# Optimization experiments

Hardware: AMD Instinct MI355X
Metric: run time of the kernel (lower is better)

The kernel has to match this reference:

```python
import jax, jax.numpy as jnp
import numpy as np

N = 100000
E = 600000
IN_DIM = 128
OUT_DIM = 256
BN_EPS = 1e-5


def setup_inputs() -> dict:
    key = jax.random.key(0)
    ks = jax.random.split(key, 12)
    x = jax.random.normal(ks[0], (N, IN_DIM), dtype=jnp.float32)
    edge_index = jax.random.randint(ks[1], (2, E), 0, N, dtype=jnp.int64)
    s1 = 1.0 / np.sqrt(IN_DIM)
    s2 = 1.0 / np.sqrt(OUT_DIM)
    return {
        "x": x,
        "edge_index": edge_index,
        "eps": jnp.zeros((), dtype=jnp.float32),  # GINConv eps init = 0
        "W1": jax.random.uniform(ks[2], (IN_DIM, OUT_DIM), jnp.float32, -s1, s1),
        "b1": jnp.zeros((OUT_DIM,), jnp.float32),
        "W2": jax.random.uniform(ks[3], (OUT_DIM, OUT_DIM), jnp.float32, -s2, s2),
        "b2": jnp.zeros((OUT_DIM,), jnp.float32),
        "gamma": jnp.ones((OUT_DIM,), jnp.float32),
        "beta": jnp.zeros((OUT_DIM,), jnp.float32),
        "run_mean": jnp.zeros((OUT_DIM,), jnp.float32),
        "run_var": jnp.ones((OUT_DIM,), jnp.float32),
        "Wp": jax.random.uniform(ks[4], (IN_DIM, OUT_DIM), jnp.float32, -s1, s1),
        "bp": jnp.zeros((OUT_DIM,), jnp.float32),
    }


def reference(x, edge_index, eps, W1, b1, W2, b2, gamma, beta, run_mean, run_var, Wp, bp):
    src, dst = edge_index[0], edge_index[1]
    # GIN aggregation: sum_{j in N(i)} x_j  (scatter-add of source features to dst)
    agg = jax.ops.segment_sum(x[src], dst, num_segments=N)
    h = (1.0 + eps) * x + agg            # [N, in_dim]
    # 2-layer MLP (nn1)
    h = jax.nn.relu(h @ W1 + b1) @ W2 + b2   # [N, out_dim]
    # BatchNorm1d (eval mode: running stats); dropout = identity (eval)
    h = (h - run_mean) * jax.lax.rsqrt(run_var + BN_EPS) * gamma + beta
    # residual with projection (in_dim != out_dim)
    return h + x @ Wp + bp
```

## Files before the change

kernel.cpp:

```cpp
#include <hip/hip_runtime.h>

#define N_ 100000
#define E_ 600000
#define IND_ 128
#define OUTD_ 256
#define NT_ (N_/16)
#define NB_ 98
#define CASTN_ (N_*IND_/2)

typedef __attribute__((ext_vector_type(8))) short bf16x8;
typedef __attribute__((ext_vector_type(4))) float f32x4;
typedef __attribute__((ext_vector_type(2))) unsigned int u32x2;

static __device__ __forceinline__ unsigned f2bf_u(float f){
  union { float f; unsigned u; } v; v.f = f;
  return (v.u + 0x7fffu + ((v.u >> 16) & 1u)) >> 16;
}
static __device__ __forceinline__ unsigned pack2(float a, float b){
  return f2bf_u(a) | (f2bf_u(b) << 16);
}
static __device__ __forceinline__ float blo(unsigned u){
  union { unsigned u; float f; } v; v.u = u << 16; return v.f;
}
static __device__ __forceinline__ float bhi(unsigned u){
  union { unsigned u; float f; } v; v.u = u & 0xffff0000u; return v.f;
}
static __device__ __forceinline__ void gload_lds16(const bf16x8* g, bf16x8* l){
  __builtin_amdgcn_global_load_lds((const __attribute__((address_space(1))) void*)g,
                                   (__attribute__((address_space(3))) void*)l, 16, 0, 0);
}

__global__ void k_prep(const float* __restrict__ x,
                       const float* __restrict__ W1, const float* __restrict__ W2,
                       const float* __restrict__ Wp, const float* __restrict__ b2,
                       const float* __restrict__ gamma, const float* __restrict__ beta,
                       const float* __restrict__ mean, const float* __restrict__ var,
                       const float* __restrict__ bp,
                       const int* __restrict__ dst, int* __restrict__ deg,
                       unsigned short* __restrict__ W1s, unsigned short* __restrict__ W2s,
                       unsigned short* __restrict__ Wps,
                       float* __restrict__ scale, float* __restrict__ shift,
                       unsigned* __restrict__ xbw)
{
  int gid = blockIdx.x*256 + threadIdx.x;
  if (gid < 16384) {
    const float* W; unsigned short* Ws; int u;
    if (gid < 4096)       { W = W1; Ws = W1s; u = gid; }
    else if (gid < 12288) { W = W2; Ws = W2s; u = gid - 4096; }
    else                  { W = Wp; Ws = Wps; u = gid - 12288; }
    int l  = u & 63;
    int km = (u >> 6) & 1;
    int t  = (u >> 7) & 15;
    int q  = u >> 11;
    int kk = 2*q + km;
    int kb = kk*32 + (l >> 4)*8;
    int c  = 16*t + (l & 15);
    #pragma unroll
    for (int j = 0; j < 8; j++)
      Ws[u*8 + j] = (unsigned short)f2bf_u(W[(size_t)(kb + j)*OUTD_ + c]);
  } else if (gid < 16640) {
    int c = gid - 16384;
    float s = gamma[c] * rsqrtf(var[c] + 1e-5f);
    scale[c] = s;
    shift[c] = (b2[c] - mean[c]) * s + beta[c] + bp[c];
  } else if (gid < 16640 + CASTN_) {
    int ci = gid - 16640;
    float2 v = ((const float2*)x)[ci];
    xbw[ci] = pack2(v.x, v.y);
  } else if (gid < 16640 + CASTN_ + E_) {
    int e = gid - 16640 - CASTN_;
    atomicAdd(&deg[dst[e]], 1);
  }
}

__global__ __launch_bounds__(1024) void k_scan1(const int* __restrict__ deg,
                                                int* __restrict__ bsum, int* __restrict__ offs){
  __shared__ int red[16];
  int tid = threadIdx.x;
  int i = blockIdx.x*1024 + tid;
  int v = (i < N_) ? deg[i] : 0;
  #pragma unroll
  for (int d = 32; d; d >>= 1) v += __shfl_down(v, d);
  if ((tid & 63) == 0) red[tid >> 6] = v;
  __syncthreads();
  if (tid < 16) {
    int s = red[tid];
    #pragma unroll
    for (int d = 8; d; d >>= 1) s += __shfl_down(s, d, 16);
    if (tid == 0) bsum[blockIdx.x] = s;
  }
  if (blockIdx.x == 0 && tid == 0) offs[N_] = E_;
}

__global__ __launch_bounds__(1024) void k_scan2(const int* __restrict__ deg,
                                                const int* __restrict__ bsum, int* __restrict__ offs){
  __shared__ int bs[128];
  __shared__ int d1[1024];
  int tid = threadIdx.x;
  if (tid < 128) bs[tid] = (tid < NB_) ? bsum[tid] : 0;
  __syncthreads();
  #pragma unroll
  for (int d = 1; d < 128; d <<= 1){
    int v = (tid < 128 && tid >= d) ? bs[tid - d] : 0;
    __syncthreads();
    if (tid < 128) bs[tid] += v;
    __syncthreads();
  }
  int bprefix = (blockIdx.x > 0) ? bs[blockIdx.x - 1] : 0;
  int i = blockIdx.x*1024 + tid;
  int v = (i < N_) ? deg[i] : 0;
  d1[tid] = v;
  __syncthreads();
  #pragma unroll
  for (int d = 1; d < 1024; d <<= 1){
    int t = (tid >= d) ? d1[tid - d] : 0;
    __syncthreads();
    d1[tid] += t;
    __syncthreads();
  }
  if (i < N_) offs[i] = bprefix + d1[tid] - v;
}

__global__ void k_fill(const int* __restrict__ src, const int* __restrict__ dst,
                       const int* __restrict__ offs, int* __restrict__ cur, int* __restrict__ adj){
  int e = blockIdx.x*256 + threadIdx.x;
  if (e < E_) {
    int d = dst[e];
    int p = atomicAdd(&cur[d], 1);
    adj[offs[d] + p] = src[e];
  }
}

__global__ void k_agg(const unsigned* __restrict__ xb32, const int* __restrict__ offs,
                      const int* __restrict__ adj, const float* __restrict__ epsp,
                      unsigned* __restrict__ h0)
{
  int row  = blockIdx.x*4 + (threadIdx.x >> 6);
  int lane = threadIdx.x & 63;
  if (row >= N_) return;
  unsigned xw = xb32[(size_t)row*64 + lane];
  float ax0=0,ay0=0,ax1=0,ay1=0,ax2=0,ay2=0,ax3=0,ay3=0;
  float ax4=0,ay4=0,ax5=0,ay5=0,ax6=0,ay6=0,ax7=0,ay7=0;
  int b = offs[row], e = offs[row+1];
  for (int base = b; base < e; base += 64){
    int cnt = min(64, e - base);
    int idx = adj[base + min(lane, cnt - 1)];
    int j = 0;
    for (; j + 8 <= cnt; j += 8){
      int n0 = __shfl(idx, j+0), n1 = __shfl(idx, j+1);
      int n2 = __shfl(idx, j+2), n3 = __shfl(idx, j+3);
      int n4 = __shfl(idx, j+4), n5 = __shfl(idx, j+5);
      int n6 = __shfl(idx, j+6), n7 = __shfl(idx, j+7);
      unsigned v0 = xb32[(size_t)n0*64 + lane];
      unsigned v1 = xb32[(size_t)n1*64 + lane];
      unsigned v2 = xb32[(size_t)n2*64 + lane];
      unsigned v3 = xb32[(size_t)n3*64 + lane];
      unsigned v4 = xb32[(size_t)n4*64 + lane];
      unsigned v5 = xb32[(size_t)n5*64 + lane];
      unsigned v6 = xb32[(size_t)n6*64 + lane];
      unsigned v7 = xb32[(size_t)n7*64 + lane];
      ax0 += blo(v0); ay0 += bhi(v0);
      ax1 += blo(v1); ay1 += bhi(v1);
      ax2 += blo(v2); ay2 += bhi(v2);
      ax3 += blo(v3); ay3 += bhi(v3);
      ax4 += blo(v4); ay4 += bhi(v4);
      ax5 += blo(v5); ay5 += bhi(v5);
      ax6 += blo(v6); ay6 += bhi(v6);
      ax7 += blo(v7); ay7 += bhi(v7);
    }
    for (; j + 4 <= cnt; j += 4){
      int n0 = __shfl(idx, j+0), n1 = __shfl(idx, j+1);
      int n2 = __shfl(idx, j+2), n3 = __shfl(idx, j+3);
      unsigned v0 = xb32[(size_t)n0*64 + lane];
      unsigned v1 = xb32[(size_t)n1*64 + lane];
      unsigned v2 = xb32[(size_t)n2*64 + lane];
      unsigned v3 = xb32[(size_t)n3*64 + lane];
      ax0 += blo(v0); ay0 += bhi(v0);
      ax1 += blo(v1); ay1 += bhi(v1);
      ax2 += blo(v2); ay2 += bhi(v2);
      ax3 += blo(v3); ay3 += bhi(v3);
    }
    if (j + 2 <= cnt){
      int n0 = __shfl(idx, j+0), n1 = __shfl(idx, j+1);
      unsigned v0 = xb32[(size_t)n0*64 + lane];
      unsigned v1 = xb32[(size_t)n1*64 + lane];
      ax4 += blo(v0); ay4 += bhi(v0);
      ax5 += blo(v1); ay5 += bhi(v1);
      j += 2;
    }
    if (j < cnt){
      int n = __shfl(idx, j);
      unsigned v = xb32[(size_t)n*64 + lane];
      ax6 += blo(v); ay6 += bhi(v);
    }
  }
  float ax = ((ax0+ax1)+(ax2+ax3)) + ((ax4+ax5)+(ax6+ax7));
  float ay = ((ay0+ay1)+(ay2+ay3)) + ((ay4+ay5)+(ay6+ay7));
  float k1 = 1.f + epsp[0];
  h0[(size_t)row*64 + lane] = pack2(fmaf(k1, blo(xw), ax), fmaf(k1, bhi(xw), ay));
}

__global__ __launch_bounds__(256) void k_mlp(const unsigned short* __restrict__ h0,
        const unsigned short* __restrict__ xb16,
        const bf16x8* __restrict__ W1s, const float* __restrict__ b1,
        const bf16x8* __restrict__ W2s, const bf16x8* __restrict__ Wps,
        const float* __restrict__ scale, const float* __restrict__ shift,
        float* __restrict__ out)
{
  __shared__ bf16x8 w[4][1024];
  __shared__ __align__(16) char trans[4][2][1280];
  int tid = threadIdx.x;
  int wv = tid >> 6, lane = tid & 63, g = lane >> 4, r = lane & 15;
  int tile0 = blockIdx.x*4 + wv;
  int tile  = min(tile0, NT_ - 1);

  const bf16x8* hrow = (const bf16x8*)(h0 + ((size_t)tile*16 + r)*IND_);
  const bf16x8* xrow = (const bf16x8*)(xb16 + ((size_t)tile*16 + r)*IND_);
  bf16x8 B[4], XV[4];
  #pragma unroll
  for (int kk = 0; kk < 4; kk++) B[kk] = hrow[kk*4 + g];
  #pragma unroll
  for (int kk = 0; kk < 4; kk++) XV[kk] = xrow[kk*4 + g];

  const bf16x8* sl[16];
  #pragma unroll
  for (int i = 0; i < 4; i++)  sl[i]      = W1s + i*1024;
  #pragma unroll
  for (int i = 0; i < 8; i++)  sl[4 + i]  = W2s + i*1024;
  #pragma unroll
  for (int i = 0; i < 4; i++)  sl[12 + i] = Wps + i*1024;

  auto STAGE = [&](int buf, const bf16x8* src){
    #pragma unroll
    for (int i = 0; i < 4; i++)
      gload_lds16(&src[i*256 + wv*64 + lane], &w[buf][i*256 + wv*64]);
  };
  f32x4 acc[16];
  auto MF16 = [&](int buf, bf16x8 f0, bf16x8 f1, int tb){
    #pragma unroll
    for (int tt = 0; tt < 8; tt++)
      acc[tb+tt] = __builtin_amdgcn_mfma_f32_16x16x32_bf16(w[buf][(tt*2+0)*64 + lane], f0, acc[tb+tt], 0,0,0);
    #pragma unroll
    for (int tt = 0; tt < 8; tt++)
      acc[tb+tt] = __builtin_amdgcn_mfma_f32_16x16x32_bf16(w[buf][(tt*2+1)*64 + lane], f1, acc[tb+tt], 0,0,0);
  };
  #pragma unroll
  for (int t = 0; t < 16; t++) acc[t] = (f32x4){0.f,0.f,0.f,0.f};

#define PHASE(P, VM, F0, F1, TB)                                   \
  { if ((P) + 2 < 16) STAGE(((P)+2)&3, sl[(P)+2]);                 \
    asm volatile("s_waitcnt vmcnt(" VM ")" ::: "memory");          \
    __builtin_amdgcn_s_barrier();                                  \
    __builtin_amdgcn_s_setprio(1);                                 \
    MF16((P)&3, F0, F1, TB);                                       \
    __builtin_amdgcn_s_setprio(0); }

  STAGE(0, sl[0]);
  STAGE(1, sl[1]);

  PHASE(0,  "8", B[0], B[1], 0)
  PHASE(1,  "8", B[0], B[1], 8)
  PHASE(2,  "8", B[2], B[3], 0)
  PHASE(3,  "8", B[2], B[3], 8)

  const float4* b1v = (const float4*)b1;
  bf16x8 H[8];
  #pragma unroll
  for (int kkh = 0; kkh < 8; kkh++){
    char* tr = &trans[wv][kkh & 1][0];
    #pragma unroll
    for (int h = 0; h < 2; h++){
      int t = 2*kkh + h;
      float4 bb = b1v[t*4 + g];
      f32x4 a = acc[t];
      float v0 = fmaxf(a.x + bb.x, 0.f);
      float v1 = fmaxf(a.y + bb.y, 0.f);
      float v2 = fmaxf(a.z + bb.z, 0.f);
      float v3 = fmaxf(a.w + bb.w, 0.f);
      u32x2 dd; dd.x = pack2(v0, v1); dd.y = pack2(v2, v3);
      *(u32x2*)(tr + r*80 + h*32 + g*8) = dd;
    }
    H[kkh] = *(const bf16x8*)(tr + r*80 + g*16);
  }
  #pragma unroll
  for (int t = 0; t < 16; t++) acc[t] = (f32x4){0.f,0.f,0.f,0.f};

  PHASE(4,  "8", H[0], H[1], 0)
  PHASE(5,  "8", H[0], H[1], 8)
  PHASE(6,  "8", H[2], H[3], 0)
  PHASE(7,  "8", H[2], H[3], 8)
  PHASE(8,  "8", H[4], H[5], 0)
  PHASE(9,  "8", H[4], H[5], 8)
  PHASE(10, "8", H[6], H[7], 0)
  PHASE(11, "8", H[6], H[7], 8)
  PHASE(12, "8", XV[0], XV[1], 0)
  PHASE(13, "8", XV[0], XV[1], 8)
  PHASE(14, "4", XV[2], XV[3], 0)
  PHASE(15, "0", XV[2], XV[3], 8)
#undef PHASE

  if (tile0 < NT_){
    const float4* sc = (const float4*)scale;
    const float4* sh = (const float4*)shift;
    #pragma unroll
    for (int t = 0; t < 16; t++){
      float4 s = sc[t*4 + g], b = sh[t*4 + g];
      f32x4 a = acc[t];
      float4 o;
      o.x = fmaf(a.x, s.x, b.x);
      o.y = fmaf(a.y, s.y, b.y);
      o.z = fmaf(a.z, s.z, b.z);
      o.w = fmaf(a.w, s.w, b.w);
      *(float4*)(out + ((size_t)tile*16 + r)*OUTD_ + t*16 + g*4) = o;
    }
  }
}

extern "C" void kernel_launch(void* const* d_in, const int* in_sizes, int n_in,
                              void* d_out, int out_size, void* d_ws, size_t ws_size,
                              hipStream_t stream)
{
  const float* x     = (const float*)d_in[0];
  const int*   ei    = (const int*)d_in[1];
  const float* eps   = (const float*)d_in[2];
  const float* W1    = (const float*)d_in[3];
  const float* b1    = (const float*)d_in[4];
  const float* W2    = (const float*)d_in[5];
  const float* b2    = (const float*)d_in[6];
  const float* gamma = (const float*)d_in[7];
  const float* beta  = (const float*)d_in[8];
  const float* rmean = (const float*)d_in[9];
  const float* rvar  = (const float*)d_in[10];
  const float* Wp    = (const float*)d_in[11];
  const float* bp    = (const float*)d_in[12];
  float* out = (float*)d_out;

  char* ws = (char*)d_ws; size_t off = 0;
  auto carve = [&](size_t b)->char* { char* p = ws + off; off = (off + b + 255) & ~(size_t)255; return p; };
  unsigned*       xbuf  = (unsigned*)carve((size_t)CASTN_*4);
  unsigned*       h0    = (unsigned*)carve((size_t)N_*64*4);
  unsigned short* W1s   = (unsigned short*)carve(4096*16);
  unsigned short* W2s   = (unsigned short*)carve(8192*16);
  unsigned short* Wps   = (unsigned short*)carve(4096*16);
  float*          scale = (float*)carve(256*4);
  float*          shift = (float*)carve(256*4);
  int*            deg   = (int*)carve((size_t)N_*4);
  int*            cur   = (int*)carve((size_t)N_*4);
  int*            offs  = (int*)carve((size_t)(N_+1)*4);
  int*            adj   = (int*)carve((size_t)E_*4);
  int*            bsum  = (int*)carve((size_t)NB_*4);

  hipMemsetAsync(deg, 0, (size_t)N_*4, stream);
  hipMemsetAsync(cur, 0, (size_t)N_*4, stream);

  k_prep <<<(16640 + CASTN_ + E_ + 255)/256, 256, 0, stream>>>(x, W1, W2, Wp, b2, gamma, beta,
                                  rmean, rvar, bp, ei + E_, deg,
                                  W1s, W2s, Wps, scale, shift, xbuf);
  k_scan1<<<NB_, 1024, 0, stream>>>(deg, bsum, offs);
  k_scan2<<<NB_, 1024, 0, stream>>>(deg, bsum, offs);
  k_fill <<<(E_+255)/256, 256, 0, stream>>>(ei, ei + E_, offs, cur, adj);
  k_agg  <<<(N_+3)/4, 256, 0, stream>>>(xbuf, offs, adj, eps, h0);
  k_mlp  <<<(NT_+3)/4, 256, 0, stream>>>((const unsigned short*)h0, (const unsigned short*)xbuf,
                                         (const bf16x8*)W1s, b1, (const bf16x8*)W2s,
                                         (const bf16x8*)Wps, scale, shift, out);
}
```

Baseline: 184.8 us.

## Process two row tiles per wave in MLP kernel to reuse staged weights

Each wave in k_mlp now computes two 16-row tiles instead of one, so every weight fragment read from LDS feeds two MFMAs. The grid is halved, which halves how often the full weight set is staged into LDS and the number of barriers per row. Loading of the x rows for the projection is moved later to reduce live registers, and launch bounds request two blocks per CU. Doubling the accumulators and fragment registers raises register pressure and may lower occupancy or cause spills.

```diff
diff --git a/kernel.cpp b/kernel.cpp
--- a/kernel.cpp
+++ b/kernel.cpp
@@ -200,7 +200,7 @@
   h0[(size_t)row*64 + lane] = pack2(fmaf(k1, blo(xw), ax), fmaf(k1, bhi(xw), ay));
 }
 
-__global__ __launch_bounds__(256) void k_mlp(const unsigned short* __restrict__ h0,
+__global__ __launch_bounds__(256, 2) void k_mlp(const unsigned short* __restrict__ h0,
         const unsigned short* __restrict__ xb16,
         const bf16x8* __restrict__ W1s, const float* __restrict__ b1,
         const bf16x8* __restrict__ W2s, const bf16x8* __restrict__ Wps,
@@ -211,16 +211,18 @@
   __shared__ __align__(16) char trans[4][2][1280];
   int tid = threadIdx.x;
   int wv = tid >> 6, lane = tid & 63, g = lane >> 4, r = lane & 15;
-  int tile0 = blockIdx.x*4 + wv;
-  int tile  = min(tile0, NT_ - 1);
-
-  const bf16x8* hrow = (const bf16x8*)(h0 + ((size_t)tile*16 + r)*IND_);
-  const bf16x8* xrow = (const bf16x8*)(xb16 + ((size_t)tile*16 + r)*IND_);
-  bf16x8 B[4], XV[4];
-  #pragma unroll
-  for (int kk = 0; kk < 4; kk++) B[kk] = hrow[kk*4 + g];
-  #pragma unroll
-  for (int kk = 0; kk < 4; kk++) XV[kk] = xrow[kk*4 + g];
+  int tA0 = blockIdx.x*8 + wv*2;
+  int tB0 = tA0 + 1;
+  int tA = min(tA0, NT_ - 1);
+  int tB = min(tB0, NT_ - 1);
+
+  const bf16x8* hrowA = (const bf16x8*)(h0 + ((size_t)tA*16 + r)*IND_);
+  const bf16x8* hrowB = (const bf16x8*)(h0 + ((size_t)tB*16 + r)*IND_);
+  bf16x8 BA[4], BB[4];
+  #pragma unroll
+  for (int kk = 0; kk < 4; kk++) BA[kk] = hrowA[kk*4 + g];
+  #pragma unroll
+  for (int kk = 0; kk < 4; kk++) BB[kk] = hrowB[kk*4 + g];
 
   const bf16x8* sl[16];
   #pragma unroll
@@ -235,8 +237,8 @@
     for (int i = 0; i < 4; i++)
       gload_lds16(&src[i*256 + wv*64 + lane], &w[buf][i*256 + wv*64]);
   };
-  f32x4 acc[16];
-  auto MF16 = [&](int buf, bf16x8 f0, bf16x8 f1, int tb){
+  f32x4 accA[16], accB[16];
+  auto MF16 = [&](int buf, bf16x8 f0, bf16x8 f1, int tb, f32x4 (&acc)[16]){
     #pragma unroll
     for (int tt = 0; tt < 8; tt++)
       acc[tb+tt] = __builtin_amdgcn_mfma_f32_16x16x32_bf16(w[buf][(tt*2+0)*64 + lane], f0, acc[tb+tt], 0,0,0);
@@ -245,73 +247,101 @@
       acc[tb+tt] = __builtin_amdgcn_mfma_f32_16x16x32_bf16(w[buf][(tt*2+1)*64 + lane], f1, acc[tb+tt], 0,0,0);
   };
   #pragma unroll
-  for (int t = 0; t < 16; t++) acc[t] = (f32x4){0.f,0.f,0.f,0.f};
-
-#define PHASE(P, VM, F0, F1, TB)                                   \
+  for (int t = 0; t < 16; t++){ accA[t] = (f32x4){0.f,0.f,0.f,0.f}; accB[t] = (f32x4){0.f,0.f,0.f,0.f}; }
+
+  const float4* b1v = (const float4*)b1;
+  auto EPI = [&](f32x4 (&acc)[16], bf16x8 (&H)[8]){
+    #pragma unroll
+    for (int kkh = 0; kkh < 8; kkh++){
+      char* tr = &trans[wv][kkh & 1][0];
+      #pragma unroll
+      for (int h = 0; h < 2; h++){
+        int t = 2*kkh + h;
+        float4 bb = b1v[t*4 + g];
+        f32x4 a = acc[t];
+        float v0 = fmaxf(a.x + bb.x, 0.f);
+        float v1 = fmaxf(a.y + bb.y, 0.f);
+        float v2 = fmaxf(a.z + bb.z, 0.f);
+        float v3 = fmaxf(a.w + bb.w, 0.f);
+        u32x2 dd; dd.x = pack2(v0, v1); dd.y = pack2(v2, v3);
+        *(u32x2*)(tr + r*80 + h*32 + g*8) = dd;
+      }
+      H[kkh] = *(const bf16x8*)(tr + r*80 + g*16);
+    }
+    #pragma unroll
+    for (int t = 0; t < 16; t++) acc[t] = (f32x4){0.f,0.f,0.f,0.f};
+  };
+
+#define PHASE(P, VM, FA0, FA1, FB0, FB1, TB)                       \
   { if ((P) + 2 < 16) STAGE(((P)+2)&3, sl[(P)+2]);                 \
     asm volatile("s_waitcnt vmcnt(" VM ")" ::: "memory");          \
     __builtin_amdgcn_s_barrier();                                  \
     __builtin_amdgcn_s_setprio(1);                                 \
-    MF16((P)&3, F0, F1, TB);                                       \
+    MF16((P)&3, FA0, FA1, TB, accA);                               \
+    MF16((P)&3, FB0, FB1, TB, accB);                               \
     __builtin_amdgcn_s_setprio(0); }
 
   STAGE(0, sl[0]);
   STAGE(1, sl[1]);
 
-  PHASE(0,  "8", B[0], B[1], 0)
-  PHASE(1,  "8", B[0], B[1], 8)
-  PHASE(2,  "8", B[2], B[3], 0)
-  PHASE(3,  "8", B[2], B[3], 8)
-
-  const float4* b1v = (const float4*)b1;
-  bf16x8 H[8];
-  #pragma unroll
-  for (int kkh = 0; kkh < 8; kkh++){
-    char* tr = &trans[wv][kkh & 1][0];
-    #pragma unroll
-    for (int h = 0; h < 2; h++){
-      int t = 2*kkh + h;
-      float4 bb = b1v[t*4 + g];
-      f32x4 a = acc[t];
-      float v0 = fmaxf(a.x + bb.x, 0.f);
-      float v1 = fmaxf(a.y + bb.y, 0.f);
-      float v2 = fmaxf(a.z + bb.z, 0.f);
-      float v3 = fmaxf(a.w + bb.w, 0.f);
-      u32x2 dd; dd.x = pack2(v0, v1); dd.y = pack2(v2, v3);
-      *(u32x2*)(tr + r*80 + h*32 + g*8) = dd;
-    }
-    H[kkh] = *(const bf16x8*)(tr + r*80 + g*16);
-  }
-  #pragma unroll
-  for (int t = 0; t < 16; t++) acc[t] = (f32x4){0.f,0.f,0.f,0.f};
-
-  PHASE(4,  "8", H[0], H[1], 0)
-  PHASE(5,  "8", H[0], H[1], 8)
-  PHASE(6,  "8", H[2], H[3], 0)
-  PHASE(7,  "8", H[2], H[3], 8)
-  PHASE(8,  "8", H[4], H[5], 0)
-  PHASE(9,  "8", H[4], H[5], 8)
-  PHASE(10, "8", H[6], H[7], 0)
-  PHASE(11, "8", H[6], H[7], 8)
-  PHASE(12, "8", XV[0], XV[1], 0)
-  PHASE(13, "8", XV[0], XV[1], 8)
-  PHASE(14, "4", XV[2], XV[3], 0)
-  PHASE(15, "0", XV[2], XV[3], 8)
+  PHASE(0,  "8", BA[0], BA[1], BB[0], BB[1], 0)
+  PHASE(1,  "8", BA[0], BA[1], BB[0], BB[1], 8)
+  PHASE(2,  "8", BA[2], BA[3], BB[2], BB[3], 0)
+  PHASE(3,  "8", BA[2], BA[3], BB[2], BB[3], 8)
+
+  bf16x8 HA[8], HB[8];
+  EPI(accA, HA);
+  EPI(accB, HB);
+
+  PHASE(4,  "8", HA[0], HA[1], HB[0], HB[1], 0)
+  PHASE(5,  "8", HA[0], HA[1], HB[0], HB[1], 8)
+  PHASE(6,  "8", HA[2], HA[3], HB[2], HB[3], 0)
+  PHASE(7,  "8", HA[2], HA[3], HB[2], HB[3], 8)
+  PHASE(8,  "8", HA[4], HA[5], HB[4], HB[5], 0)
+  PHASE(9,  "8", HA[4], HA[5], HB[4], HB[5], 8)
+
+  const bf16x8* xrowA = (const bf16x8*)(xb16 + ((size_t)tA*16 + r)*IND_);
+  const bf16x8* xrowB = (const bf16x8*)(xb16 + ((size_t)tB*16 + r)*IND_);
+  bf16x8 XA[4], XB[4];
+  #pragma unroll
+  for (int kk = 0; kk < 4; kk++) XA[kk] = xrowA[kk*4 + g];
+  #pragma unroll
+  for (int kk = 0; kk < 4; kk++) XB[kk] = xrowB[kk*4 + g];
+
+  PHASE(10, "8", HA[6], HA[7], HB[6], HB[7], 0)
+  PHASE(11, "8", HA[6], HA[7], HB[6], HB[7], 8)
+  PHASE(12, "8", XA[0], XA[1], XB[0], XB[1], 0)
+  PHASE(13, "8", XA[0], XA[1], XB[0], XB[1], 8)
+  PHASE(14, "4", XA[2], XA[3], XB[2], XB[3], 0)
+  PHASE(15, "0", XA[2], XA[3], XB[2], XB[3], 8)
 #undef PHASE
 
-  if (tile0 < NT_){
-    const float4* sc = (const float4*)scale;
-    const float4* sh = (const float4*)shift;
+  const float4* sc = (const float4*)scale;
+  const float4* sh = (const float4*)shift;
+  if (tA0 < NT_){
     #pragma unroll
     for (int t = 0; t < 16; t++){
       float4 s = sc[t*4 + g], b = sh[t*4 + g];
-      f32x4 a = acc[t];
+      f32x4 a = accA[t];
       float4 o;
       o.x = fmaf(a.x, s.x, b.x);
       o.y = fmaf(a.y, s.y, b.y);
       o.z = fmaf(a.z, s.z, b.z);
       o.w = fmaf(a.w, s.w, b.w);
-      *(float4*)(out + ((size_t)tile*16 + r)*OUTD_ + t*16 + g*4) = o;
+      *(float4*)(out + ((size_t)tA*16 + r)*OUTD_ + t*16 + g*4) = o;
+    }
+  }
+  if (tB0 < NT_){
+    #pragma unroll
+    for (int t = 0; t < 16; t++){
+      float4 s = sc[t*4 + g], b = sh[t*4 + g];
+      f32x4 a = accB[t];
+      float4 o;
+      o.x = fmaf(a.x, s.x, b.x);
+      o.y = fmaf(a.y, s.y, b.y);
+      o.z = fmaf(a.z, s.z, b.z);
+      o.w = fmaf(a.w, s.w, b.w);
+      *(float4*)(out + ((size_t)tB*16 + r)*OUTD_ + t*16 + g*4) = o;
     }
   }
 }
@@ -360,7 +390,7 @@
   k_scan2<<<NB_, 1024, 0, stream>>>(deg, bsum, offs);
   k_fill <<<(E_+255)/256, 256, 0, stream>>>(ei, ei + E_, offs, cur, adj);
   k_agg  <<<(N_+3)/4, 256, 0, stream>>>(xbuf, offs, adj, eps, h0);
-  k_mlp  <<<(NT_+3)/4, 256, 0, stream>>>((const unsigned short*)h0, (const unsigned short*)xbuf,
+  k_mlp  <<<(NT_+7)/8, 256, 0, stream>>>((const unsigned short*)h0, (const unsigned short*)xbuf,
                                          (const bf16x8*)W1s, b1, (const bf16x8*)W2s,
                                          (const bf16x8*)Wps, scale, shift, out);
 }
```

After: 186.2 us. Within noise of the previous version (+0.7%).
